# Performance work log

Hardware: AMD Instinct MI355X
Metric: run time of the kernel (lower is better)

The kernel has to match this reference:

```python
import jax, jax.numpy as jnp
import numpy as np

B = 65536   # collocation batch
D = 8       # total_dim (tokens)
H = 128     # subnet hidden_dim
E = 64      # attn_embed_dim == subnet output_dim (proj is None)
NH = 4      # attention heads
GA = 4      # groupA_size


def setup_inputs() -> dict:
    key = jax.random.key(0)
    ks = iter(jax.random.split(key, 32))
    n = lambda shape, s: jax.random.normal(next(ks), shape, dtype=jnp.float32) * s
    inp = {
        "x":  jax.random.normal(next(ks), (B, D), dtype=jnp.float32),
        "w1": n((D, H), 1.0),                 # Lin(1,H) per dim (xavier ~ sqrt(2/(1+H)))
        "b1": jnp.zeros((D, H), jnp.float32),
        "w2": n((D, H, H), 1.0 / np.sqrt(H)),
        "b2": jnp.zeros((D, H), jnp.float32),
        "w3": n((D, E, H), 1.0 / np.sqrt(H)),
        "b3": jnp.zeros((D, E), jnp.float32),
    }
    for tag in ("sa", "sb", "ca", "cb"):
        inp[f"Win_{tag}"] = n((3 * E, E), 1.0 / np.sqrt(E))
        inp[f"bin_{tag}"] = jnp.zeros((3 * E,), jnp.float32)
        inp[f"Wo_{tag}"]  = n((E, E), 1.0 / np.sqrt(E))
        inp[f"bo_{tag}"]  = jnp.zeros((E,), jnp.float32)
    inp["Wf"] = n((1, 2 * E), 1.0 / np.sqrt(2 * E))
    inp["bf"] = jnp.zeros((1,), jnp.float32)
    return inp


def _mha(q, k, v, Win, bin_, Wo, bo):
    # PyTorch nn.MultiheadAttention (batch_first=True) math
    Wq, Wk, Wv = jnp.split(Win, 3, axis=0)
    bq, bk, bv = jnp.split(bin_, 3)
    dh = E // NH
    def heads(t, W, b):
        p = t @ W.T + b                         # [B,S,E]
        return p.reshape(p.shape[0], p.shape[1], NH, dh)
    qh = heads(q, Wq, bq)
    kh = heads(k, Wk, bk)
    vh = heads(v, Wv, bv)
    att = jnp.einsum('bqhd,bkhd->bhqk', qh, kh) / jnp.sqrt(jnp.float32(dh))
    w = jax.nn.softmax(att, axis=-1)
    o = jnp.einsum('bhqk,bkhd->bqhd', w, vh)
    o = o.reshape(o.shape[0], o.shape[1], E)
    return o @ Wo.T + bo


def reference(x, w1, b1, w2, b2, w3, b3,
              Win_sa, bin_sa, Wo_sa, bo_sa,
              Win_sb, bin_sb, Wo_sb, bo_sb,
              Win_ca, bin_ca, Wo_ca, bo_ca,
              Win_cb, bin_cb, Wo_cb, bo_cb,
              Wf, bf):
    # Per-dim subnets as block-diagonal batched matmuls (activation='sin', dropout=0)
    h = jnp.sin(x[:, :, None] * w1[None] + b1[None])            # [B,D,H]
    h = jnp.sin(jnp.einsum('bdh,dkh->bdk', h, w2) + b2[None])   # [B,D,H]
    tokens = jnp.einsum('bdh,doh->bdo', h, w3) + b3[None]       # [B,D,E]

    A = tokens[:, :GA, :]
    Bt = tokens[:, GA:, :]
    A_self  = _mha(A,  A,  A,  Win_sa, bin_sa, Wo_sa, bo_sa)
    B_self  = _mha(Bt, Bt, Bt, Win_sb, bin_sb, Wo_sb, bo_sb)
    A_cross = _mha(A,  Bt, Bt, Win_ca, bin_ca, Wo_ca, bo_ca)
    B_cross = _mha(Bt, A,  A,  Win_cb, bin_cb, Wo_cb, bo_cb)

    A_pool = ((A_self + A_cross) * 0.5).mean(axis=1)            # [B,E]
    B_pool = ((B_self + B_cross) * 0.5).mean(axis=1)            # [B,E]
    combined = jnp.concatenate([A_pool, B_pool], axis=1)        # [B,2E]
    out = combined @ Wf.T + bf                                  # [B,1]
    return jax.nn.leaky_relu(out, 0.01)
```

## Files before the change

### kernel.cpp

```cpp
#include <hip/hip_runtime.h>

typedef unsigned short u16;
typedef __attribute__((ext_vector_type(8))) short short8;
typedef __attribute__((ext_vector_type(4))) short s16x4;
typedef __attribute__((ext_vector_type(4))) float f32x4;
typedef __attribute__((ext_vector_type(2))) unsigned int u32x2;

#define OFF_U     0
#define OFF_CV    1024
#define OFF_CONST 1040
#define OFF_CTAG  1044
#define OFF_BA    1056
#define OFF_BB    1328
#define OFF_WA_B    6400
#define OFF_WB_B    41216
#define OFF_W2P_B   76032
#define OFF_W3P_B   338176
#define OFF_TOK_B   469248

#define P_STRIDE 280
#define PSIDE    (32 * P_STRIDE)

static __device__ __forceinline__ u16 f2bf(float f) {
  unsigned int bits = __float_as_uint(f);
  bits += 0x7fffu + ((bits >> 16) & 1u);
  return (u16)(bits >> 16);
}
static __device__ __forceinline__ unsigned rbits(float f) {
  unsigned b = __float_as_uint(f);
  return b + 0x7fffu + ((b >> 16) & 1u);
}
static __device__ __forceinline__ float bf2f(u16 u) {
  return __uint_as_float(((unsigned int)u) << 16);
}

__global__ __launch_bounds__(64) void prep_fold(
    const float* __restrict__ win_sa, const float* __restrict__ bin_sa,
    const float* __restrict__ wo_sa,  const float* __restrict__ bo_sa,
    const float* __restrict__ win_sb, const float* __restrict__ bin_sb,
    const float* __restrict__ wo_sb,  const float* __restrict__ bo_sb,
    const float* __restrict__ win_ca, const float* __restrict__ bin_ca,
    const float* __restrict__ wo_ca,  const float* __restrict__ bo_ca,
    const float* __restrict__ win_cb, const float* __restrict__ bin_cb,
    const float* __restrict__ wo_cb,  const float* __restrict__ bo_cb,
    const float* __restrict__ Wf, float* __restrict__ ws) {
  __shared__ float v_lds[64];
  const int t = threadIdx.x;
  const int tag = blockIdx.x;
  const float* wins[4] = {win_sa, win_sb, win_ca, win_cb};
  const float* bins[4] = {bin_sa, bin_sb, bin_ca, bin_cb};
  const float* wos[4]  = {wo_sa, wo_sb, wo_ca, wo_cb};
  const float* bos[4]  = {bo_sa, bo_sb, bo_ca, bo_cb};
  const float* wfh = Wf + ((tag == 0 || tag == 2) ? 0 : 64);
  float v = 0.f;
#pragma unroll
  for (int e = 0; e < 64; e++) v += wos[tag][e * 64 + t] * wfh[e];
  v_lds[t] = v;
  __syncthreads();
#pragma unroll
  for (int h = 0; h < 4; h++) {
    float u = 0.f;
#pragma unroll
    for (int dp = 0; dp < 16; dp++)
      u += wins[tag][(128 + h * 16 + dp) * 64 + t] * v_lds[h * 16 + dp];
    ws[OFF_U + tag * 256 + h * 64 + t] = u;
  }
  if (t < 4) {
    float cv = 0.f;
#pragma unroll
    for (int dp = 0; dp < 16; dp++)
      cv += bins[tag][128 + t * 16 + dp] * v_lds[t * 16 + dp];
    ws[OFF_CV + tag * 4 + t] = cv;
  }
  if (t == 0) {
    float c = 0.f;
#pragma unroll
    for (int e = 0; e < 64; e++) c += bos[tag][e] * wfh[e];
    ws[OFF_CTAG + tag] = c;
  }
}

__global__ __launch_bounds__(256) void prep_pack(
    const float* __restrict__ w2, const float* __restrict__ w3,
    const float* __restrict__ win_sa, const float* __restrict__ win_sb,
    const float* __restrict__ win_ca, const float* __restrict__ win_cb,
    const float* __restrict__ bin_sa, const float* __restrict__ bin_sb,
    const float* __restrict__ bin_ca, const float* __restrict__ bin_cb,
    const float* __restrict__ bf,
    float* __restrict__ ws, u16* __restrict__ w2p, u16* __restrict__ w3p,
    u16* __restrict__ WA, u16* __restrict__ WB) {
  int idx = blockIdx.x * 256 + threadIdx.x;
  if (idx < 131072) {
    int d = idx >> 14, rem = idx & 16383;
    int f = rem >> 9, ks = f >> 3, nt = f & 7;
    int r2 = rem & 511, l = r2 >> 3, j = r2 & 7;
    int quad = l >> 4, m15 = l & 15;
    w2p[idx] = f2bf(w2[(d * 128 + nt * 16 + m15) * 128 + ks * 32 + quad * 8 + j]);
  } else if (idx < 196608) {
    int i = idx - 131072;
    int d = i >> 13, rem = i & 8191;
    int f = rem >> 9, ks = f >> 2, nt = f & 3;
    int r2 = rem & 511, l = r2 >> 3, j = r2 & 7;
    int quad = l >> 4, m15 = l & 15;
    w3p[i] = f2bf(w3[(d * 64 + nt * 16 + m15) * 128 + ks * 32 + quad * 8 + j]);
  } else if (idx < 214016) {
    int i = idx - 196608;
    int nt = i >> 10, rem = i & 1023;
    int half = rem >> 9, r2 = rem & 511, l = r2 >> 3, j = r2 & 7;
    int n = nt * 16 + (l & 15), k = half * 32 + (l >> 4) * 8 + j;
    float v;
    if (n < 64)       v = win_sa[n * 64 + k] * 0.25f;
    else if (n < 128) v = win_sa[n * 64 + k];
    else if (n < 192) v = win_ca[(n - 128) * 64 + k] * 0.25f;
    else if (n < 256) v = win_cb[(n - 128) * 64 + k];
    else if (n < 260) v = ws[OFF_U + 0 * 256 + (n - 256) * 64 + k];
    else if (n < 264) v = ws[OFF_U + 3 * 256 + (n - 260) * 64 + k];
    else              v = 0.f;
    WA[i] = f2bf(v);
  } else if (idx < 231424) {
    int i = idx - 214016;
    int nt = i >> 10, rem = i & 1023;
    int half = rem >> 9, r2 = rem & 511, l = r2 >> 3, j = r2 & 7;
    int n = nt * 16 + (l & 15), k = half * 32 + (l >> 4) * 8 + j;
    float v;
    if (n < 64)       v = win_sb[n * 64 + k] * 0.25f;
    else if (n < 128) v = win_sb[n * 64 + k];
    else if (n < 192) v = win_cb[(n - 128) * 64 + k] * 0.25f;
    else if (n < 256) v = win_ca[(n - 128) * 64 + k];
    else if (n < 260) v = ws[OFF_U + 1 * 256 + (n - 256) * 64 + k];
    else if (n < 264) v = ws[OFF_U + 2 * 256 + (n - 260) * 64 + k];
    else              v = 0.f;
    WB[i] = f2bf(v);
  } else if (idx < 231696) {
    int n = idx - 231424;
    float v;
    if (n < 64)       v = bin_sa[n] * 0.25f;
    else if (n < 128) v = bin_sa[n];
    else if (n < 192) v = bin_ca[n - 128] * 0.25f;
    else if (n < 256) v = bin_cb[n - 128];
    else if (n < 260) v = ws[OFF_CV + 0 * 4 + (n - 256)];
    else if (n < 264) v = ws[OFF_CV + 3 * 4 + (n - 260)];
    else              v = 0.f;
    ws[OFF_BA + n] = v;
  } else if (idx < 231968) {
    int n = idx - 231696;
    float v;
    if (n < 64)       v = bin_sb[n] * 0.25f;
    else if (n < 128) v = bin_sb[n];
    else if (n < 192) v = bin_cb[n - 128] * 0.25f;
    else if (n < 256) v = bin_ca[n - 128];
    else if (n < 260) v = ws[OFF_CV + 1 * 4 + (n - 256)];
    else if (n < 264) v = ws[OFF_CV + 2 * 4 + (n - 260)];
    else              v = 0.f;
    ws[OFF_BB + n] = v;
  } else if (idx == 231968) {
    ws[OFF_CONST] = 0.5f * (ws[OFF_CTAG] + ws[OFF_CTAG + 1] +
                            ws[OFF_CTAG + 2] + ws[OFF_CTAG + 3]) + bf[0];
  }
}

__global__ __launch_bounds__(256, 4) void tokens_kernel(
    const float* __restrict__ x, const float* __restrict__ w1,
    const float* __restrict__ b1, const float* __restrict__ b2,
    const float* __restrict__ b3, const u16* __restrict__ w2p,
    const u16* __restrict__ w3p, u16* __restrict__ tok_out) {
  __shared__ __align__(16) u16 scratch[4][32 * 136];
  const int t = threadIdx.x;
  const int wave = t >> 6, lane = t & 63;
  const int m15 = lane & 15, quad = lane >> 4;
  const int d = blockIdx.x >> 9;
  const int g = blockIdx.x & 511;
  const int b0 = g * 128 + wave * 32;
  const float xv0 = x[(size_t)(b0 + m15) * 8 + d];
  const float xv1 = x[(size_t)(b0 + 16 + m15) * 8 + d];

  const u16* w2base = w2p + d * 16384 + lane * 8;
  f32x4 acc2[2][8];
#pragma unroll
  for (int mt = 0; mt < 2; mt++)
#pragma unroll
    for (int nt = 0; nt < 8; nt++) acc2[mt][nt] = (f32x4){0.f, 0.f, 0.f, 0.f};
#pragma unroll
  for (int ks = 0; ks < 4; ks++) {
    const float* w1p = w1 + d * 128 + ks * 32 + quad * 8;
    const float* b1p = b1 + d * 128 + ks * 32 + quad * 8;
    float4 wa = *(const float4*)w1p, wb = *(const float4*)(w1p + 4);
    float4 ba = *(const float4*)b1p, bb = *(const float4*)(b1p + 4);
    short8 a0, a1;
    a0[0] = (short)f2bf(__sinf(xv0 * wa.x + ba.x));
    a0[1] = (short)f2bf(__sinf(xv0 * wa.y + ba.y));
    a0[2] = (short)f2bf(__sinf(xv0 * wa.z + ba.z));
    a0[3] = (short)f2bf(__sinf(xv0 * wa.w + ba.w));
    a0[4] = (short)f2bf(__sinf(xv0 * wb.x + bb.x));
    a0[5] = (short)f2bf(__sinf(xv0 * wb.y + bb.y));
    a0[6] = (short)f2bf(__sinf(xv0 * wb.z + bb.z));
    a0[7] = (short)f2bf(__sinf(xv0 * wb.w + bb.w));
    a1[0] = (short)f2bf(__sinf(xv1 * wa.x + ba.x));
    a1[1] = (short)f2bf(__sinf(xv1 * wa.y + ba.y));
    a1[2] = (short)f2bf(__sinf(xv1 * wa.z + ba.z));
    a1[3] = (short)f2bf(__sinf(xv1 * wa.w + ba.w));
    a1[4] = (short)f2bf(__sinf(xv1 * wb.x + bb.x));
    a1[5] = (short)f2bf(__sinf(xv1 * wb.y + bb.y));
    a1[6] = (short)f2bf(__sinf(xv1 * wb.z + bb.z));
    a1[7] = (short)f2bf(__sinf(xv1 * wb.w + bb.w));
#pragma unroll
    for (int nt = 0; nt < 8; nt++) {
      short8 bfr = *(const short8*)(w2base + (ks * 8 + nt) * 512);
      acc2[0][nt] = __builtin_amdgcn_mfma_f32_16x16x32_bf16(bfr, a0, acc2[0][nt], 0, 0, 0);
      acc2[1][nt] = __builtin_amdgcn_mfma_f32_16x16x32_bf16(bfr, a1, acc2[1][nt], 0, 0, 0);
    }
  }
#pragma unroll
  for (int nt = 0; nt < 8; nt++) {
    float4 bi = *(const float4*)(b2 + d * 128 + nt * 16 + quad * 4);
#pragma unroll
    for (int mt = 0; mt < 2; mt++) {
      u32x2 pk;
      pk[0] = (rbits(__sinf(acc2[mt][nt][1] + bi.y)) & 0xffff0000u) |
              (rbits(__sinf(acc2[mt][nt][0] + bi.x)) >> 16);
      pk[1] = (rbits(__sinf(acc2[mt][nt][3] + bi.w)) & 0xffff0000u) |
              (rbits(__sinf(acc2[mt][nt][2] + bi.z)) >> 16);
      *(u32x2*)&scratch[wave][(mt * 16 + m15) * 136 + nt * 16 + quad * 4] = pk;
    }
  }
  const u16* w3base = w3p + d * 8192 + lane * 8;
  f32x4 acc3[2][4];
#pragma unroll
  for (int mt = 0; mt < 2; mt++)
#pragma unroll
    for (int nt = 0; nt < 4; nt++) acc3[mt][nt] = (f32x4){0.f, 0.f, 0.f, 0.f};
#pragma unroll
  for (int ks = 0; ks < 4; ks++) {
    short8 af0 = *(const short8*)&scratch[wave][m15 * 136 + ks * 32 + quad * 8];
    short8 af1 = *(const short8*)&scratch[wave][(16 + m15) * 136 + ks * 32 + quad * 8];
#pragma unroll
    for (int nt = 0; nt < 4; nt++) {
      short8 bfr = *(const short8*)(w3base + (ks * 4 + nt) * 512);
      acc3[0][nt] = __builtin_amdgcn_mfma_f32_16x16x32_bf16(bfr, af0, acc3[0][nt], 0, 0, 0);
      acc3[1][nt] = __builtin_amdgcn_mfma_f32_16x16x32_bf16(bfr, af1, acc3[1][nt], 0, 0, 0);
    }
  }
#pragma unroll
  for (int nt = 0; nt < 4; nt++) {
    float4 bi = *(const float4*)(b3 + d * 64 + nt * 16 + quad * 4);
#pragma unroll
    for (int mt = 0; mt < 2; mt++) {
      u32x2 pk;
      pk[0] = (rbits(acc3[mt][nt][1] + bi.y) & 0xffff0000u) |
              (rbits(acc3[mt][nt][0] + bi.x) >> 16);
      pk[1] = (rbits(acc3[mt][nt][3] + bi.w) & 0xffff0000u) |
              (rbits(acc3[mt][nt][2] + bi.z) >> 16);
      *(u32x2*)&scratch[wave][(mt * 16 + m15) * 136 + nt * 16 + quad * 4] = pk;
    }
  }
  {
    int chunk = lane & 7;
#pragma unroll
    for (int it = 0; it < 4; it++) {
      int row_l = (lane >> 3) + it * 8;
      short8 v = *(const short8*)&scratch[wave][row_l * 136 + chunk * 8];
      *(short8*)(tok_out + ((size_t)(d * 65536 + b0 + row_l)) * 64 + chunk * 8) = v;
    }
  }
}

__global__ __launch_bounds__(128, 4) void attn_kernel(
    const float* __restrict__ ws, const u16* __restrict__ tok,
    const u16* __restrict__ WA, const u16* __restrict__ WB,
    float* __restrict__ out) {
  __shared__ __align__(16) u16 P[2 * PSIDE];
  const int t = threadIdx.x;
  const int wave = t >> 6, lane = t & 63;
  const int m15 = lane & 15, quad = lane >> 4;
  const int side = wave;
  const int b0 = blockIdx.x * 8;
  const float cst = ws[OFF_CONST];

  {
    const u16* W = side ? WB : WA;
    const float* bias = ws + (side ? OFF_BB : OFF_BA);
    const int dd = (m15 & 3) + side * 4;
    short8 a0[2], a1[2];
#pragma unroll
    for (int mt = 0; mt < 2; mt++) {
      const int e = mt * 4 + (m15 >> 2);
      const u16* ab = tok + ((size_t)(dd * 65536 + b0 + e)) * 64 + quad * 8;
      a0[mt] = *(const short8*)ab;
      a1[mt] = *(const short8*)(ab + 32);
    }
    u16* Pb = &P[side * PSIDE];
#pragma unroll
    for (int nt = 0; nt < 17; nt++) {
      const u16* bp = W + nt * 1024 + lane * 8;
      short8 w0f = *(const short8*)bp;
      short8 w1f = *(const short8*)(bp + 512);
      float4 bi = *(const float4*)(bias + nt * 16 + quad * 4);
#pragma unroll
      for (int mt = 0; mt < 2; mt++) {
        f32x4 acc = {0.f, 0.f, 0.f, 0.f};
        acc = __builtin_amdgcn_mfma_f32_16x16x32_bf16(w0f, a0[mt], acc, 0, 0, 0);
        acc = __builtin_amdgcn_mfma_f32_16x16x32_bf16(w1f, a1[mt], acc, 0, 0, 0);
        u32x2 pk;
        pk[0] = (rbits(acc[1] + bi.y) & 0xffff0000u) | (rbits(acc[0] + bi.x) >> 16);
        pk[1] = (rbits(acc[3] + bi.w) & 0xffff0000u) | (rbits(acc[2] + bi.z) >> 16);
        *(u32x2*)&Pb[(mt * 16 + m15) * P_STRIDE + nt * 16 + quad * 4] = pk;
      }
    }
  }
  __syncthreads();
  {
    const int eg = wave;
    const int q2 = (quad & 1) * 8;
    const bool hiq = (quad & 2) != 0;
    const u16* row0 = P + (size_t)(eg * 16 + m15) * P_STRIDE;
    const u16* row1 = row0 + PSIDE;
    float acc = 0.f;
#pragma unroll
    for (int tag = 0; tag < 4; tag++) {
      const int qs = tag & 1, cross = tag >> 1;
      const int ks2 = qs ^ cross;
      const u16* rowK = ks2 ? row1 : row0;
      const u16* rowQ = qs ? row1 : row0;
      const u16* vbase = P + ks2 * PSIDE +
                         (size_t)(eg * 16 + quad * 4) * P_STRIDE + 256 + cross * 4;
      s16x4 vv0 = *(const s16x4*)(vbase);
      s16x4 vv1 = *(const s16x4*)(vbase + P_STRIDE);
      s16x4 vv2 = *(const s16x4*)(vbase + 2 * P_STRIDE);
      s16x4 vv3 = *(const s16x4*)(vbase + 3 * P_STRIDE);
#pragma unroll
      for (int h = 0; h < 4; h++) {
        const int kcol = 64 + cross * 128 + h * 16 + q2;
        const int qcol = hiq ? 264 : (cross * 128 + h * 16 + q2);
        short8 afr = *(const short8*)(rowK + kcol);
        short8 bfr = *(const short8*)(rowQ + qcol);
        f32x4 c = {0.f, 0.f, 0.f, 0.f};
        c = __builtin_amdgcn_mfma_f32_16x16x32_bf16(afr, bfr, c, 0, 0, 0);
        float e0 = __expf(c[0]), e1 = __expf(c[1]);
        float e2 = __expf(c[2]), e3 = __expf(c[3]);
        float o = e0 * bf2f((u16)vv0[h]) + e1 * bf2f((u16)vv1[h]) +
                  e2 * bf2f((u16)vv2[h]) + e3 * bf2f((u16)vv3[h]);
        acc += o * __builtin_amdgcn_rcpf(e0 + e1 + e2 + e3);
      }
    }
    acc += __shfl_xor(acc, 1);
    acc += __shfl_xor(acc, 2);
    if (quad == (m15 >> 2) && (m15 & 3) == 0) {
      float val = 0.125f * acc + cst;
      out[b0 + eg * 4 + quad] = val > 0.f ? val : 0.01f * val;
    }
  }
}

extern "C" void kernel_launch(void* const* d_in, const int* in_sizes, int n_in,
                              void* d_out, int out_size, void* d_ws, size_t ws_size,
                              hipStream_t stream) {
  const float* x      = (const float*)d_in[0];
  const float* w1     = (const float*)d_in[1];
  const float* b1     = (const float*)d_in[2];
  const float* w2     = (const float*)d_in[3];
  const float* b2     = (const float*)d_in[4];
  const float* w3     = (const float*)d_in[5];
  const float* b3     = (const float*)d_in[6];
  const float* win_sa = (const float*)d_in[7];
  const float* bin_sa = (const float*)d_in[8];
  const float* wo_sa  = (const float*)d_in[9];
  const float* bo_sa  = (const float*)d_in[10];
  const float* win_sb = (const float*)d_in[11];
  const float* bin_sb = (const float*)d_in[12];
  const float* wo_sb  = (const float*)d_in[13];
  const float* bo_sb  = (const float*)d_in[14];
  const float* win_ca = (const float*)d_in[15];
  const float* bin_ca = (const float*)d_in[16];
  const float* wo_ca  = (const float*)d_in[17];
  const float* bo_ca  = (const float*)d_in[18];
  const float* win_cb = (const float*)d_in[19];
  const float* bin_cb = (const float*)d_in[20];
  const float* wo_cb  = (const float*)d_in[21];
  const float* bo_cb  = (const float*)d_in[22];
  const float* Wf     = (const float*)d_in[23];
  const float* bf     = (const float*)d_in[24];
  float* ws = (float*)d_ws;
  u16* WAp    = (u16*)((char*)d_ws + OFF_WA_B);
  u16* WBp    = (u16*)((char*)d_ws + OFF_WB_B);
  u16* w2p    = (u16*)((char*)d_ws + OFF_W2P_B);
  u16* w3p    = (u16*)((char*)d_ws + OFF_W3P_B);
  u16* tokbuf = (u16*)((char*)d_ws + OFF_TOK_B);
  float* out = (float*)d_out;

  prep_fold<<<4, 64, 0, stream>>>(win_sa, bin_sa, wo_sa, bo_sa,
                                  win_sb, bin_sb, wo_sb, bo_sb,
                                  win_ca, bin_ca, wo_ca, bo_ca,
                                  win_cb, bin_cb, wo_cb, bo_cb,
                                  Wf, ws);
  prep_pack<<<907, 256, 0, stream>>>(w2, w3, win_sa, win_sb, win_ca, win_cb,
                                     bin_sa, bin_sb, bin_ca, bin_cb, bf,
                                     ws, w2p, w3p, WAp, WBp);
  tokens_kernel<<<4096, 256, 0, stream>>>(x, w1, b1, b2, b3, w2p, w3p, tokbuf);
  attn_kernel<<<8192, 128, 0, stream>>>(ws, tokbuf, WAp, WBp, out);
}
```

Baseline: 208.8 us.

## Double attn block batch, split projection tiles across waves, keep V in fp32 LDS

The attention kernel now handles 16 batch rows per block with 4 waves instead of 8 rows with 2 waves. The two waves on each side split the 17 projection column tiles between them (9 each, with tile 8 computed by both), which halves the per-wave serial projection work and amortises the weight-fragment loads over more rows. Packing to bf16 uses the hardware v_cvt_pk_bf16_f32 instruction instead of manual rounding. The folded V values are also kept in fp32 in a separate LDS array, which removes the bf16 unpacking in the softmax loop and slightly changes numerics. In exchange, LDS per block grows and occupancy is capped at 2 blocks of 256 threads.

```diff
diff --git a/kernel.cpp b/kernel.cpp
--- a/kernel.cpp
+++ b/kernel.cpp
@@ -19,7 +19,7 @@
 #define OFF_TOK_B   469248
 
 #define P_STRIDE 280
-#define PSIDE    (32 * P_STRIDE)
+#define PSIDE2   (64 * P_STRIDE)
 
 static __device__ __forceinline__ u16 f2bf(float f) {
   unsigned int bits = __float_as_uint(f);
@@ -30,8 +30,10 @@
   unsigned b = __float_as_uint(f);
   return b + 0x7fffu + ((b >> 16) & 1u);
 }
-static __device__ __forceinline__ float bf2f(u16 u) {
-  return __uint_as_float(((unsigned int)u) << 16);
+static __device__ __forceinline__ unsigned cvtpk(float lo, float hi) {
+  unsigned r;
+  asm("v_cvt_pk_bf16_f32 %0, %1, %2" : "=v"(r) : "v"(lo), "v"(hi));
+  return r;
 }
 
 __global__ __launch_bounds__(64) void prep_fold(
@@ -264,46 +266,52 @@
   }
 }
 
-__global__ __launch_bounds__(128, 4) void attn_kernel(
+__global__ __launch_bounds__(256, 2) void attn_kernel(
     const float* __restrict__ ws, const u16* __restrict__ tok,
     const u16* __restrict__ WA, const u16* __restrict__ WB,
     float* __restrict__ out) {
-  __shared__ __align__(16) u16 P[2 * PSIDE];
+  __shared__ __align__(16) u16 P[2 * PSIDE2];
+  __shared__ __align__(16) float Vf[2][64][12];
   const int t = threadIdx.x;
   const int wave = t >> 6, lane = t & 63;
   const int m15 = lane & 15, quad = lane >> 4;
-  const int side = wave;
-  const int b0 = blockIdx.x * 8;
+  const int b0 = blockIdx.x * 16;
   const float cst = ws[OFF_CONST];
 
   {
+    const int side = wave & 1, nh = wave >> 1;
     const u16* W = side ? WB : WA;
     const float* bias = ws + (side ? OFF_BB : OFF_BA);
     const int dd = (m15 & 3) + side * 4;
-    short8 a0[2], a1[2];
-#pragma unroll
-    for (int mt = 0; mt < 2; mt++) {
+    short8 a0[4], a1[4];
+#pragma unroll
+    for (int mt = 0; mt < 4; mt++) {
       const int e = mt * 4 + (m15 >> 2);
       const u16* ab = tok + ((size_t)(dd * 65536 + b0 + e)) * 64 + quad * 8;
       a0[mt] = *(const short8*)ab;
       a1[mt] = *(const short8*)(ab + 32);
     }
-    u16* Pb = &P[side * PSIDE];
-#pragma unroll
-    for (int nt = 0; nt < 17; nt++) {
+    u16* Pb = &P[side * PSIDE2];
+#pragma unroll
+    for (int i = 0; i < 9; i++) {
+      const int nt = nh ? (8 + i) : i;
       const u16* bp = W + nt * 1024 + lane * 8;
       short8 w0f = *(const short8*)bp;
       short8 w1f = *(const short8*)(bp + 512);
       float4 bi = *(const float4*)(bias + nt * 16 + quad * 4);
 #pragma unroll
-      for (int mt = 0; mt < 2; mt++) {
+      for (int mt = 0; mt < 4; mt++) {
         f32x4 acc = {0.f, 0.f, 0.f, 0.f};
         acc = __builtin_amdgcn_mfma_f32_16x16x32_bf16(w0f, a0[mt], acc, 0, 0, 0);
         acc = __builtin_amdgcn_mfma_f32_16x16x32_bf16(w1f, a1[mt], acc, 0, 0, 0);
+        float v0 = acc[0] + bi.x, v1 = acc[1] + bi.y;
+        float v2 = acc[2] + bi.z, v3 = acc[3] + bi.w;
         u32x2 pk;
-        pk[0] = (rbits(acc[1] + bi.y) & 0xffff0000u) | (rbits(acc[0] + bi.x) >> 16);
-        pk[1] = (rbits(acc[3] + bi.w) & 0xffff0000u) | (rbits(acc[2] + bi.z) >> 16);
+        pk[0] = cvtpk(v0, v1);
+        pk[1] = cvtpk(v2, v3);
         *(u32x2*)&Pb[(mt * 16 + m15) * P_STRIDE + nt * 16 + quad * 4] = pk;
+        if (i == 8 && nh && quad < 2)
+          *(float4*)&Vf[side][mt * 16 + m15][quad * 4] = (float4){v0, v1, v2, v3};
       }
     }
   }
@@ -313,7 +321,7 @@
     const int q2 = (quad & 1) * 8;
     const bool hiq = (quad & 2) != 0;
     const u16* row0 = P + (size_t)(eg * 16 + m15) * P_STRIDE;
-    const u16* row1 = row0 + PSIDE;
+    const u16* row1 = row0 + PSIDE2;
     float acc = 0.f;
 #pragma unroll
     for (int tag = 0; tag < 4; tag++) {
@@ -321,12 +329,14 @@
       const int ks2 = qs ^ cross;
       const u16* rowK = ks2 ? row1 : row0;
       const u16* rowQ = qs ? row1 : row0;
-      const u16* vbase = P + ks2 * PSIDE +
-                         (size_t)(eg * 16 + quad * 4) * P_STRIDE + 256 + cross * 4;
-      s16x4 vv0 = *(const s16x4*)(vbase);
-      s16x4 vv1 = *(const s16x4*)(vbase + P_STRIDE);
-      s16x4 vv2 = *(const s16x4*)(vbase + 2 * P_STRIDE);
-      s16x4 vv3 = *(const s16x4*)(vbase + 3 * P_STRIDE);
+      float4 vv0 = *(const float4*)&Vf[ks2][eg * 16 + quad * 4 + 0][cross * 4];
+      float4 vv1 = *(const float4*)&Vf[ks2][eg * 16 + quad * 4 + 1][cross * 4];
+      float4 vv2 = *(const float4*)&Vf[ks2][eg * 16 + quad * 4 + 2][cross * 4];
+      float4 vv3 = *(const float4*)&Vf[ks2][eg * 16 + quad * 4 + 3][cross * 4];
+      float vvs[4][4] = {{vv0.x, vv0.y, vv0.z, vv0.w},
+                         {vv1.x, vv1.y, vv1.z, vv1.w},
+                         {vv2.x, vv2.y, vv2.z, vv2.w},
+                         {vv3.x, vv3.y, vv3.z, vv3.w}};
 #pragma unroll
       for (int h = 0; h < 4; h++) {
         const int kcol = 64 + cross * 128 + h * 16 + q2;
@@ -337,8 +347,8 @@
         c = __builtin_amdgcn_mfma_f32_16x16x32_bf16(afr, bfr, c, 0, 0, 0);
         float e0 = __expf(c[0]), e1 = __expf(c[1]);
         float e2 = __expf(c[2]), e3 = __expf(c[3]);
-        float o = e0 * bf2f((u16)vv0[h]) + e1 * bf2f((u16)vv1[h]) +
-                  e2 * bf2f((u16)vv2[h]) + e3 * bf2f((u16)vv3[h]);
+        float o = e0 * vvs[0][h] + e1 * vvs[1][h] +
+                  e2 * vvs[2][h] + e3 * vvs[3][h];
         acc += o * __builtin_amdgcn_rcpf(e0 + e1 + e2 + e3);
       }
     }
@@ -396,5 +406,5 @@
                                      bin_sa, bin_sb, bin_ca, bin_cb, bf,
                                      ws, w2p, w3p, WAp, WBp);
   tokens_kernel<<<4096, 256, 0, stream>>>(x, w1, b1, b2, b3, w2p, w3p, tokbuf);
-  attn_kernel<<<8192, 128, 0, stream>>>(ws, tokbuf, WAp, WBp, out);
-}
+  attn_kernel<<<4096, 256, 0, stream>>>(ws, tokbuf, WAp, WBp, out);
+}
```

After: 202.0 us. 1.03x faster.
